# Kernel optimization log

Measured on AMD Instinct MI355X. Metric: run time of the kernel, lower is better.

## Reference

```python
import jax, jax.numpy as jnp
import numpy as np

B, N, D, H, L, C = 64, 64, 64, 256, 64, 2


def setup_inputs() -> dict:
    key = jax.random.key(0)
    ks = iter(jax.random.split(key, 40))

    def p(*shape):
        return (jax.random.normal(next(ks), shape, jnp.float32) / np.sqrt(shape[0])).astype(jnp.float32)

    inp = {
        "x": jax.random.normal(next(ks), (B, N, D), jnp.float32),
        "adj": jax.random.uniform(next(ks), (B, N, N), jnp.float32),
        "condition": jax.random.normal(next(ks), (B, C), jnp.float32),
        # GraphConv layers
        "gc1_W": p(D, H), "gc1_b": jnp.zeros((H,)),
        "gc2_W": p(H, H), "gc2_b": jnp.zeros((H,)),
        "gc3mu_W": p(H, L), "gc3mu_b": jnp.zeros((L,)),
        "gc3lv_W": p(H, L), "gc3lv_b": jnp.zeros((L,)),
        # condition encoder
        "ce_W1": p(C, H), "ce_b1": jnp.zeros((H,)),
        "ce_W2": p(H, H), "ce_b2": jnp.zeros((H,)),
        # decoder
        "dec_W1": p(L + H, H), "dec_b1": jnp.zeros((H,)),
        "dec_W2": p(H, H), "dec_b2": jnp.zeros((H,)),
        "dec_W3": p(H, D), "dec_b3": jnp.zeros((D,)),
        # atom type predictor
        "at_W1": p(D, H), "at_b1": jnp.zeros((H,)),
        "at_W2": p(H, 8), "at_b2": jnp.zeros((8,)),
        # bond predictor
        "bp_W1": p(2 * D + H, H), "bp_b1": jnp.zeros((H,)),
        "bp_W2": p(H, H), "bp_b2": jnp.zeros((H,)),
        "bp_W3": p(H, 4), "bp_b3": jnp.zeros((4,)),
        # rule encoder
        "re_W1": p(D, H), "re_b1": jnp.zeros((H,)),
        "re_W2": p(H, 4), "re_b2": jnp.zeros((4,)),
    }
    return inp


def reference(x, adj, condition,
              gc1_W, gc1_b, gc2_W, gc2_b, gc3mu_W, gc3mu_b, gc3lv_W, gc3lv_b,
              ce_W1, ce_b1, ce_W2, ce_b2,
              dec_W1, dec_b1, dec_W2, dec_b2, dec_W3, dec_b3,
              at_W1, at_b1, at_W2, at_b2,
              bp_W1, bp_b1, bp_W2, bp_b2, bp_W3, bp_b3,
              re_W1, re_b1, re_W2, re_b2):
    relu = jax.nn.relu

    def gc(h, W, b):  # batched GraphConv: adj @ h then linear
        return jnp.einsum('bij,bjd->bid', adj, h) @ W + b

    # encode
    h = relu(gc(x, gc1_W, gc1_b))
    h = relu(gc(h, gc2_W, gc2_b))
    mu = gc(h, gc3mu_W, gc3mu_b)        # [B,N,L]
    logvar = gc(h, gc3lv_W, gc3lv_b)    # [B,N,L]
    z = mu  # eval-mode reparameterize (deterministic)

    # decode: condition encoding broadcast over nodes
    cond = relu(condition @ ce_W1 + ce_b1) @ ce_W2 + ce_b2  # [B,H]
    dec_in = jnp.concatenate([z, jnp.broadcast_to(cond[:, None, :], (z.shape[0], z.shape[1], cond.shape[-1]))], axis=-1)
    f = relu(dec_in @ dec_W1 + dec_b1)
    f = relu(f @ dec_W2 + dec_b2)
    features = jax.nn.sigmoid(f @ dec_W3 + dec_b3)  # [B,N,D]

    type_probs = jax.nn.softmax(relu(features @ at_W1 + at_b1) @ at_W2 + at_b2, axis=-1)  # [B,N,8]
    valence = jax.nn.sigmoid(relu(features @ re_W1 + re_b1) @ re_W2 + re_b2) * 4.0        # [B,N,4]
    atom_features = features * jnp.mean(type_probs, axis=-1, keepdims=True)               # [B,N,D]

    # dense pairwise bond probabilities (vectorized version of the per-pair MLP)
    b, n, d = atom_features.shape
    af_i = jnp.broadcast_to(atom_features[:, :, None, :], (b, n, n, d))
    af_j = jnp.broadcast_to(atom_features[:, None, :, :], (b, n, n, d))
    cnd = jnp.broadcast_to(cond[:, None, None, :], (b, n, n, cond.shape[-1]))
    pair = jnp.concatenate([af_i, af_j, cnd], axis=-1)  # [B,N,N,2D+H]
    g = relu(pair @ bp_W1 + bp_b1)
    g = relu(g @ bp_W2 + bp_b2)
    bond_probs = jax.nn.softmax(g @ bp_W3 + bp_b3, axis=-1)  # [B,N,N,4]

    return (atom_features, bond_probs, valence, mu, logvar)
```

## Files before the change

kernel.cpp:

```cpp
#include <hip/hip_runtime.h>

typedef short short8 __attribute__((ext_vector_type(8)));
typedef float f32x4 __attribute__((ext_vector_type(4)));
typedef unsigned short u16;
typedef unsigned int u32;

__device__ __forceinline__ u16 f2bf(float f) {
  union { float f; u32 u; } x; x.f = f;
  u32 u = x.u;
  u32 r = (u + 0x7FFFu + ((u >> 16) & 1u)) >> 16;
  return (u16)r;
}

__device__ __forceinline__ u32 cvtpk(float lo, float hi) {
  u32 r;
  asm("v_cvt_pk_bf16_f32 %0, %1, %2" : "=v"(r) : "v"(lo), "v"(hi));
  return r;
}

#define OW2T   0
#define OW3TX  65536
#define ODW1A  69632
#define ODW2   86016
#define ODW3   151552
#define OBPA   167936
#define OBPB   184320
#define OREW1  200704
#define OREW2  217088
#define OWMU   221184
#define OWLV   237568

__global__ void __launch_bounds__(512) k_prep(
    const float* __restrict__ cnd, const float* __restrict__ ceW1,
    const float* __restrict__ ceb1, const float* __restrict__ ceW2,
    const float* __restrict__ ceb2, const float* __restrict__ bpW1,
    const float* __restrict__ bpb1, const float* __restrict__ dW1,
    const float* __restrict__ db1, const float* __restrict__ dW2,
    const float* __restrict__ dW3, const float* __restrict__ bpW2,
    const float* __restrict__ bpW3, const float* __restrict__ reW1,
    const float* __restrict__ reW2, const float* __restrict__ gmuW,
    const float* __restrict__ glvW, float* __restrict__ ctf,
    float* __restrict__ ctv, u16* __restrict__ WB) {
  __shared__ float h[256], c2s[256], prf[256], prv[256];
  __shared__ float T[64][65];
  int bid = blockIdx.x, t = threadIdx.x;
  if (bid < 64) {
    int b = bid;
    if (t < 256) {
      float c0 = cnd[b * 2 + 0], c1 = cnd[b * 2 + 1];
      h[t] = fmaxf(c0 * ceW1[t] + c1 * ceW1[256 + t] + ceb1[t], 0.f);
    }
    __syncthreads();
    int col = t & 255, g = t >> 8;
    {
      float acc = 0.f;
      #pragma unroll 8
      for (int k = g * 128; k < g * 128 + 128; k++) acc += h[k] * ceW2[k * 256 + col];
      if (g) prf[col] = acc;
      __syncthreads();
      if (!g) c2s[col] = acc + prf[col] + ceb2[col];
    }
    __syncthreads();
    float af = 0.f, av = 0.f;
    #pragma unroll 4
    for (int k = g * 128; k < g * 128 + 128; k++) {
      float cv = c2s[k];
      af += cv * bpW1[(128 + k) * 256 + col];
      av += cv * dW1[(64 + k) * 256 + col];
    }
    if (g) { prf[col] = af; prv[col] = av; }
    __syncthreads();
    if (!g) {
      ctf[b * 256 + col] = af + prf[col] + bpb1[col];
      ctv[b * 256 + col] = av + prv[col] + db1[col];
    }
    return;
  }
  int mb = bid - 64;
  if (mb >= 60) {
    if (t < 256) {
      const float* s = (mb == 60) ? reW2 : bpW3;
      u16* d = WB + ((mb == 60) ? OREW2 : OW3TX);
      #pragma unroll
      for (int c = 0; c < 16; c++) {
        float v = (c < 4) ? s[t * 4 + c] : 0.f;
        d[c * 256 + t] = f2bf(v);
      }
    }
    return;
  }
  const float* src; u16* dst; int sld, dld, tr, tc; float sc = 1.f;
  if (mb < 4)       { src = dW1;           dst = WB + ODW1A; sld = 256; dld = 64;  tr = 0;            tc = mb;          }
  else if (mb < 20) { int e = mb - 4;  src = dW2;  dst = WB + ODW2; sld = 256; dld = 256; tr = e >> 2; tc = e & 3; }
  else if (mb < 24) { int e = mb - 20; src = dW3;  dst = WB + ODW3; sld = 64;  dld = 256; tr = e;      tc = 0;     }
  else if (mb < 28) { int e = mb - 24; src = bpW1; dst = WB + OBPA; sld = 256; dld = 64;  tr = 0;      tc = e; sc = 0.125f; }
  else if (mb < 32) { int e = mb - 28; src = bpW1 + 64 * 256; dst = WB + OBPB; sld = 256; dld = 64; tr = 0; tc = e; sc = 0.125f; }
  else if (mb < 36) { int e = mb - 32; src = reW1; dst = WB + OREW1; sld = 256; dld = 64; tr = 0;      tc = e;     }
  else if (mb < 40) { int e = mb - 36; src = gmuW; dst = WB + OWMU; sld = 64;  dld = 256; tr = e;      tc = 0;     }
  else if (mb < 44) { int e = mb - 40; src = glvW; dst = WB + OWLV; sld = 64;  dld = 256; tr = e;      tc = 0;     }
  else              { int e = mb - 44; src = bpW2; dst = WB + OW2T; sld = 256; dld = 256; tr = e >> 2; tc = e & 3; }
  int rl = t >> 6, cl = t & 63;
  #pragma unroll
  for (int it = 0; it < 8; it++) {
    int r = it * 8 + rl;
    T[r][cl] = src[(tr * 64 + r) * sld + tc * 64 + cl] * sc;
  }
  __syncthreads();
  #pragma unroll
  for (int it = 0; it < 8; it++) {
    int c2_ = it * 8 + rl;
    dst[(tc * 64 + c2_) * dld + tr * 64 + cl] = f2bf(T[cl][c2_]);
  }
}

__global__ void __launch_bounds__(512) k_gc1(
    const float* __restrict__ adj, const float* __restrict__ x,
    const float* __restrict__ W1, const float* __restrict__ b1,
    float* __restrict__ out) {
  __shared__ float adj_s[64 * 64];
  __shared__ float x_s[64 * 64];
  __shared__ float ax_s[64 * 64];
  __shared__ float h_s[64 * 64];
  int cg = blockIdx.x, b = blockIdx.y, t = threadIdx.x;
  const float* A = adj + b * 4096;
  const float* X = x + b * 4096;
  for (int e = t; e < 4096; e += 512) { adj_s[e] = A[e]; x_s[e] = X[e]; }
  __syncthreads();
  int c = t & 63, rg = t >> 6;
  {
    float acc[8];
    #pragma unroll
    for (int m = 0; m < 8; m++) acc[m] = 0.f;
    #pragma unroll 4
    for (int j4 = 0; j4 < 16; j4++) {
      float xv0 = x_s[(j4 * 4 + 0) * 64 + c];
      float xv1 = x_s[(j4 * 4 + 1) * 64 + c];
      float xv2 = x_s[(j4 * 4 + 2) * 64 + c];
      float xv3 = x_s[(j4 * 4 + 3) * 64 + c];
      #pragma unroll
      for (int m = 0; m < 8; m++) {
        float4 a4 = *(const float4*)&adj_s[(m * 8 + rg) * 64 + j4 * 4];
        acc[m] += a4.x * xv0 + a4.y * xv1 + a4.z * xv2 + a4.w * xv3;
      }
    }
    #pragma unroll
    for (int m = 0; m < 8; m++) ax_s[(m * 8 + rg) * 64 + c] = acc[m];
  }
  __syncthreads();
  {
    float bv = b1[cg * 64 + c];
    float acc[8];
    #pragma unroll
    for (int m = 0; m < 8; m++) acc[m] = bv;
    #pragma unroll 4
    for (int k4 = 0; k4 < 16; k4++) {
      float w0 = W1[(k4 * 4 + 0) * 256 + cg * 64 + c];
      float w1 = W1[(k4 * 4 + 1) * 256 + cg * 64 + c];
      float w2 = W1[(k4 * 4 + 2) * 256 + cg * 64 + c];
      float w3 = W1[(k4 * 4 + 3) * 256 + cg * 64 + c];
      #pragma unroll
      for (int m = 0; m < 8; m++) {
        float4 a4 = *(const float4*)&ax_s[(m * 8 + rg) * 64 + k4 * 4];
        acc[m] += a4.x * w0 + a4.y * w1 + a4.z * w2 + a4.w * w3;
      }
    }
    #pragma unroll
    for (int m = 0; m < 8; m++) h_s[(m * 8 + rg) * 64 + c] = fmaxf(acc[m], 0.f);
  }
  __syncthreads();
  {
    float acc[8];
    #pragma unroll
    for (int m = 0; m < 8; m++) acc[m] = 0.f;
    #pragma unroll 4
    for (int j4 = 0; j4 < 16; j4++) {
      float h0 = h_s[(j4 * 4 + 0) * 64 + c];
      float h1 = h_s[(j4 * 4 + 1) * 64 + c];
      float h2 = h_s[(j4 * 4 + 2) * 64 + c];
      float h3 = h_s[(j4 * 4 + 3) * 64 + c];
      #pragma unroll
      for (int m = 0; m < 8; m++) {
        float4 a4 = *(const float4*)&adj_s[(m * 8 + rg) * 64 + j4 * 4];
        acc[m] += a4.x * h0 + a4.y * h1 + a4.z * h2 + a4.w * h3;
      }
    }
    float* O = out + b * 64 * 256 + cg * 64;
    #pragma unroll
    for (int m = 0; m < 8; m++) O[(m * 8 + rg) * 256 + c] = acc[m];
  }
}

__global__ void __launch_bounds__(512) k_linadj(
    const float* __restrict__ adj, const float* __restrict__ in,
    const float* __restrict__ W, const float* __restrict__ bias,
    float* __restrict__ out) {
  __shared__ float adj_s[64 * 64];
  __shared__ float in_s[32 * 256];
  __shared__ float h_s[64 * 64];
  int cg = blockIdx.x, b = blockIdx.y, t = threadIdx.x;
  const float* A = adj + b * 4096;
  for (int e = t; e < 4096; e += 512) adj_s[e] = A[e];
  int c = t & 63, rg = t >> 6;
  float bv = bias[cg * 64 + c];
  #pragma unroll
  for (int half = 0; half < 2; half++) {
    if (half) __syncthreads();
    const float* I = in + (b * 64 + half * 32) * 256;
    for (int e = t; e < 32 * 256; e += 512) in_s[e] = I[e];
    __syncthreads();
    float acc[4];
    #pragma unroll
    for (int m = 0; m < 4; m++) acc[m] = bv;
    #pragma unroll 4
    for (int k4 = 0; k4 < 64; k4++) {
      float w0 = W[(k4 * 4 + 0) * 256 + cg * 64 + c];
      float w1 = W[(k4 * 4 + 1) * 256 + cg * 64 + c];
      float w2 = W[(k4 * 4 + 2) * 256 + cg * 64 + c];
      float w3 = W[(k4 * 4 + 3) * 256 + cg * 64 + c];
      #pragma unroll
      for (int m = 0; m < 4; m++) {
        float4 i4 = *(const float4*)&in_s[(m * 8 + rg) * 256 + k4 * 4];
        acc[m] += i4.x * w0 + i4.y * w1 + i4.z * w2 + i4.w * w3;
      }
    }
    #pragma unroll
    for (int m = 0; m < 4; m++)
      h_s[(half * 32 + m * 8 + rg) * 64 + c] = fmaxf(acc[m], 0.f);
  }
  __syncthreads();
  {
    float acc[8];
    #pragma unroll
    for (int m = 0; m < 8; m++) acc[m] = 0.f;
    #pragma unroll 4
    for (int j4 = 0; j4 < 16; j4++) {
      float h0 = h_s[(j4 * 4 + 0) * 64 + c];
      float h1 = h_s[(j4 * 4 + 1) * 64 + c];
      float h2 = h_s[(j4 * 4 + 2) * 64 + c];
      float h3 = h_s[(j4 * 4 + 3) * 64 + c];
      #pragma unroll
      for (int m = 0; m < 8; m++) {
        float4 a4 = *(const float4*)&adj_s[(m * 8 + rg) * 64 + j4 * 4];
        acc[m] += a4.x * h0 + a4.y * h1 + a4.z * h2 + a4.w * h3;
      }
    }
    float* O = out + b * 64 * 256 + cg * 64;
    #pragma unroll
    for (int m = 0; m < 8; m++) O[(m * 8 + rg) * 256 + c] = acc[m];
  }
}

template <int KK, int WU, int WV, bool UG, bool VG, int ULEN, int VLEN>
__device__ __forceinline__ void mmrun(const u16* __restrict__ Up, int Uoff,
                                      const u16* __restrict__ Vp, int Voff,
                                      const char* lds, int ut0, int vt0, int lr, int lk,
                                      f32x4 (&acc)[WU][WV]) {
  #pragma unroll
  for (int kk = 0; kk < KK; kk++) {
    short8 uf[WU], vf[WV];
    #pragma unroll
    for (int i = 0; i < WU; i++) {
      int row = (ut0 + i) * 16 + lr;
      if constexpr (UG) {
        uf[i] = *(const short8*)(Up + row * ULEN + kk * 32 + lk * 8);
      } else {
        int byt = Uoff + row * (ULEN * 2) + kk * 64 + lk * 16;
        byt ^= (row & 7) << 4;
        uf[i] = *(const short8*)(lds + byt);
      }
    }
    #pragma unroll
    for (int j = 0; j < WV; j++) {
      int row = (vt0 + j) * 16 + lr;
      if constexpr (VG) {
        vf[j] = *(const short8*)(Vp + row * VLEN + kk * 32 + lk * 8);
      } else {
        int byt = Voff + row * (VLEN * 2) + kk * 64 + lk * 16;
        byt ^= (row & 7) << 4;
        vf[j] = *(const short8*)(lds + byt);
      }
    }
    #pragma unroll
    for (int i = 0; i < WU; i++)
      #pragma unroll
      for (int j = 0; j < WV; j++)
        acc[i][j] = __builtin_amdgcn_mfma_f32_16x16x32_bf16(uf[i], vf[j], acc[i][j], 0, 0, 0);
  }
}

__device__ __forceinline__ void st64(char* lds, int off, int rowlen, int crow, int ccol0,
                                     float a0, float a1, float a2, float a3) {
  uint2 pk; pk.x = cvtpk(a0, a1); pk.y = cvtpk(a2, a3);
  int byt = off + crow * (rowlen * 2) + ccol0 * 2;
  byt ^= (crow & 7) << 4;
  *(uint2*)(lds + byt) = pk;
}

template <int WU, int WV>
__device__ __forceinline__ void zacc(f32x4 (&acc)[WU][WV]) {
  #pragma unroll
  for (int i = 0; i < WU; i++)
    #pragma unroll
    for (int j = 0; j < WV; j++) acc[i][j] = (f32x4){0.f, 0.f, 0.f, 0.f};
}

__global__ void __launch_bounds__(1024) k_chain2(
    const u16* __restrict__ WB, const float* __restrict__ ah2_g,
    const float* __restrict__ ctv, const float* __restrict__ ctf,
    const float* __restrict__ gmub, const float* __restrict__ glvb,
    const float* __restrict__ db2, const float* __restrict__ db3,
    const float* __restrict__ reb1, const float* __restrict__ reb2,
    float* __restrict__ mu_out, float* __restrict__ lv_out,
    float* __restrict__ af_out, float* __restrict__ val_out,
    float* __restrict__ P, float* __restrict__ Q) {
  __shared__ char L[65536];
  constexpr int S2 = 0, S3 = 32768;
  int b = blockIdx.x, t = threadIdx.x;
  int w = t >> 6, lane = t & 63, lr = lane & 15, lk = lane >> 4;

  {
    int r = t >> 4, cb = (t & 15) * 16;
    #pragma unroll
    for (int q = 0; q < 4; q++) {
      float4 v = *(const float4*)(ah2_g + ((b * 64 + r) * 256 + cb + q * 4));
      st64(L, S2, 256, r, cb + q * 4, v.x, v.y, v.z, v.w);
    }
  }
  __syncthreads();
  {
    f32x4 a[2][1]; zacc(a);
    int sel = w >> 3, wq = w & 7;
    int ut0 = (wq & 1) * 2, vt = wq >> 1;
    const u16* Up = WB + (sel ? OWLV : OWMU);
    mmrun<8, 2, 1, true, false, 256, 256>(Up, 0, WB, S2, L, ut0, vt, lr, lk, a);
    int crow = vt * 16 + lr;
    const float* bb = sel ? glvb : gmub;
    float* gout = sel ? lv_out : mu_out;
    #pragma unroll
    for (int i = 0; i < 2; i++) {
      int cc = (ut0 + i) * 16 + lk * 4;
      float4 bv = *(const float4*)(bb + cc);
      float o0 = a[i][0][0] + bv.x, o1 = a[i][0][1] + bv.y;
      float o2 = a[i][0][2] + bv.z, o3 = a[i][0][3] + bv.w;
      *(float4*)(gout + ((b * 64 + crow) * 64 + cc)) = make_float4(o0, o1, o2, o3);
      if (sel == 0) st64(L, S3, 64, crow, cc, o0, o1, o2, o3);
    }
  }
  __syncthreads();
  {
    f32x4 a[2][2]; zacc(a);
    int ut0 = (w & 7) * 2, vt0 = (w >> 3) * 2;
    mmrun<2, 2, 2, true, false, 64, 64>(WB + ODW1A, 0, WB, S3, L, ut0, vt0, lr, lk, a);
    #pragma unroll
    for (int j = 0; j < 2; j++) {
      int crow = (vt0 + j) * 16 + lr;
      #pragma unroll
      for (int i = 0; i < 2; i++) {
        int cc = (ut0 + i) * 16 + lk * 4;
        float4 cv = *(const float4*)(ctv + b * 256 + cc);
        st64(L, S2, 256, crow, cc, fmaxf(a[i][j][0] + cv.x, 0.f), fmaxf(a[i][j][1] + cv.y, 0.f),
             fmaxf(a[i][j][2] + cv.z, 0.f), fmaxf(a[i][j][3] + cv.w, 0.f));
      }
    }
  }
  __syncthreads();
  {
    f32x4 a[2][2]; zacc(a);
    int ut0 = (w & 7) * 2, vt0 = (w >> 3) * 2;
    mmrun<8, 2, 2, true, false, 256, 256>(WB + ODW2, 0, WB, S2, L, ut0, vt0, lr, lk, a);
    #pragma unroll
    for (int j = 0; j < 2; j++) {
      int crow = (vt0 + j) * 16 + lr;
      #pragma unroll
      for (int i = 0; i < 2; i++) {
        int cc = (ut0 + i) * 16 + lk * 4;
        float4 bv = *(const float4*)(db2 + cc);
        st64(L, S3, 256, crow, cc, fmaxf(a[i][j][0] + bv.x, 0.f), fmaxf(a[i][j][1] + bv.y, 0.f),
             fmaxf(a[i][j][2] + bv.z, 0.f), fmaxf(a[i][j][3] + bv.w, 0.f));
      }
    }
  }
  __syncthreads();
  {
    f32x4 a[1][1]; zacc(a);
    int ut = w & 3, vt = w >> 2;
    mmrun<8, 1, 1, true, false, 256, 256>(WB + ODW3, 0, WB, S3, L, ut, vt, lr, lk, a);
    int crow = vt * 16 + lr, cc = ut * 16 + lk * 4;
    float4 bv = *(const float4*)(db3 + cc);
    float s0 = 1.f / (1.f + expf(-(a[0][0][0] + bv.x)));
    float s1 = 1.f / (1.f + expf(-(a[0][0][1] + bv.y)));
    float s2 = 1.f / (1.f + expf(-(a[0][0][2] + bv.z)));
    float s3 = 1.f / (1.f + expf(-(a[0][0][3] + bv.w)));
    *(float4*)(af_out + ((b * 64 + crow) * 64 + cc)) =
        make_float4(s0 * 0.125f, s1 * 0.125f, s2 * 0.125f, s3 * 0.125f);
    st64(L, S2, 64, crow, cc, s0, s1, s2, s3);
  }
  __syncthreads();
  {
    f32x4 a[2][4]; zacc(a);
    int ut0 = (w & 7) * 2;
    int sel = w >> 3;
    const u16* Up = WB + (sel ? OBPB : OBPA);
    mmrun<2, 2, 4, true, false, 64, 64>(Up, 0, WB, S2, L, ut0, 0, lr, lk, a);
    float* out = sel ? Q : P;
    #pragma unroll
    for (int i = 0; i < 2; i++) {
      int cc = (ut0 + i) * 16 + lk * 4;
      float4 cv = make_float4(0.f, 0.f, 0.f, 0.f);
      if (sel == 0) cv = *(const float4*)(ctf + b * 256 + cc);
      #pragma unroll
      for (int j = 0; j < 4; j++) {
        int crow = j * 16 + lr;
        *(float4*)(out + ((b * 64 + crow) * 256 + cc)) =
            make_float4(a[i][j][0] + cv.x, a[i][j][1] + cv.y, a[i][j][2] + cv.z, a[i][j][3] + cv.w);
      }
    }
  }
  {
    f32x4 a[2][2]; zacc(a);
    int ut0 = (w & 7) * 2, vt0 = (w >> 3) * 2;
    mmrun<2, 2, 2, true, false, 64, 64>(WB + OREW1, 0, WB, S2, L, ut0, vt0, lr, lk, a);
    #pragma unroll
    for (int j = 0; j < 2; j++) {
      int crow = (vt0 + j) * 16 + lr;
      #pragma unroll
      for (int i = 0; i < 2; i++) {
        int cc = (ut0 + i) * 16 + lk * 4;
        float4 bv = *(const float4*)(reb1 + cc);
        st64(L, S3, 256, crow, cc, fmaxf(a[i][j][0] + bv.x, 0.f), fmaxf(a[i][j][1] + bv.y, 0.f),
             fmaxf(a[i][j][2] + bv.z, 0.f), fmaxf(a[i][j][3] + bv.w, 0.f));
      }
    }
  }
  __syncthreads();
  if (w < 4) {
    f32x4 a[1][1]; zacc(a);
    mmrun<8, 1, 1, true, false, 256, 256>(WB + OREW2, 0, WB, S3, L, 0, w, lr, lk, a);
    if (lk == 0) {
      float4 rb = *(const float4*)reb2;
      float v0 = 4.f / (1.f + expf(-(a[0][0][0] + rb.x)));
      float v1 = 4.f / (1.f + expf(-(a[0][0][1] + rb.y)));
      float v2 = 4.f / (1.f + expf(-(a[0][0][2] + rb.z)));
      float v3 = 4.f / (1.f + expf(-(a[0][0][3] + rb.w)));
      *(float4*)(val_out + (b * 64 + w * 16 + lr) * 4) = make_float4(v0, v1, v2, v3);
    }
  }
}

__global__ void __launch_bounds__(512, 4) k_bond(
    const float* __restrict__ P, const float* __restrict__ Q,
    const u16* __restrict__ W2T, const float* __restrict__ b2,
    const u16* __restrict__ W3Tx, const float* __restrict__ b3,
    float* __restrict__ bp_out) {
  __shared__ u16 G[2 * 64 * 256];
  int flat = blockIdx.x;
  int xcd = flat & 7, rest = flat >> 3;
  int b = xcd * 8 + (rest >> 5);
  int i0 = (rest & 31) * 2;
  int t = threadIdx.x;
  int lane = t & 63, w = t >> 6;
  int lr = lane & 15, lk = lane >> 4;

  {
    int colg = t & 63, rq = t >> 6;
    const float* Pb = P + (b * 64 + i0) * 256 + colg * 4;
    float4 p0 = *(const float4*)(Pb);
    float4 p1 = *(const float4*)(Pb + 256);
    const float* Qb = Q + b * 64 * 256;
    #pragma unroll
    for (int r = rq * 8; r < rq * 8 + 8; r++) {
      float4 q4 = *(const float4*)(Qb + r * 256 + colg * 4);
      int byt = (r * 512 + colg * 8) ^ ((r & 7) << 4);
      uint2 pk0, pk1;
      pk0.x = cvtpk(fmaxf(p0.x + q4.x, 0.f), fmaxf(p0.y + q4.y, 0.f));
      pk0.y = cvtpk(fmaxf(p0.z + q4.z, 0.f), fmaxf(p0.w + q4.w, 0.f));
      pk1.x = cvtpk(fmaxf(p1.x + q4.x, 0.f), fmaxf(p1.y + q4.y, 0.f));
      pk1.y = cvtpk(fmaxf(p1.z + q4.z, 0.f), fmaxf(p1.w + q4.w, 0.f));
      *(uint2*)((char*)G + byt) = pk0;
      *(uint2*)((char*)G + 32768 + byt) = pk1;
    }
  }
  __syncthreads();

  f32x4 acc[2][2][4];
  #pragma unroll
  for (int tl = 0; tl < 2; tl++)
    #pragma unroll
    for (int ni = 0; ni < 2; ni++)
      #pragma unroll
      for (int mi = 0; mi < 4; mi++) acc[tl][ni][mi] = (f32x4){0.f, 0.f, 0.f, 0.f};

  const u16* Wl = W2T + (w * 32 + lr) * 256 + lk * 8;
  short8 bwc0 = *(const short8*)(Wl);
  short8 bwc1 = *(const short8*)(Wl + 16 * 256);
  for (int kk = 0; kk < 8; kk++) {
    int kn = (kk + 1) & 7;
    short8 bwn0 = *(const short8*)(Wl + kn * 32);
    short8 bwn1 = *(const short8*)(Wl + 16 * 256 + kn * 32);
    __builtin_amdgcn_s_setprio(1);
    #pragma unroll
    for (int mi = 0; mi < 4; mi++) {
      int row = mi * 16 + lr;
      int byt = (row * 512 + kk * 64 + lk * 16) ^ ((row & 7) << 4);
      short8 a0 = *(const short8*)((const char*)G + byt);
      short8 a1 = *(const short8*)((const char*)G + 32768 + byt);
      acc[0][0][mi] = __builtin_amdgcn_mfma_f32_16x16x32_bf16(bwc0, a0, acc[0][0][mi], 0, 0, 0);
      acc[1][0][mi] = __builtin_amdgcn_mfma_f32_16x16x32_bf16(bwc0, a1, acc[1][0][mi], 0, 0, 0);
      acc[0][1][mi] = __builtin_amdgcn_mfma_f32_16x16x32_bf16(bwc1, a0, acc[0][1][mi], 0, 0, 0);
      acc[1][1][mi] = __builtin_amdgcn_mfma_f32_16x16x32_bf16(bwc1, a1, acc[1][1][mi], 0, 0, 0);
    }
    __builtin_amdgcn_s_setprio(0);
    bwc0 = bwn0;
    bwc1 = bwn1;
  }
  __syncthreads();

  #pragma unroll
  for (int tl = 0; tl < 2; tl++)
    #pragma unroll
    for (int ni = 0; ni < 2; ni++) {
      int col0 = w * 32 + ni * 16 + lk * 4;
      float4 bb = *(const float4*)(b2 + col0);
      #pragma unroll
      for (int mi = 0; mi < 4; mi++) {
        int grow = mi * 16 + lr;
        uint2 pk;
        pk.x = cvtpk(fmaxf(acc[tl][ni][mi][0] + bb.x, 0.f), fmaxf(acc[tl][ni][mi][1] + bb.y, 0.f));
        pk.y = cvtpk(fmaxf(acc[tl][ni][mi][2] + bb.z, 0.f), fmaxf(acc[tl][ni][mi][3] + bb.w, 0.f));
        int byt = ((grow * 512 + col0 * 2) ^ ((grow & 7) << 4)) + tl * 32768;
        *(uint2*)((char*)G + byt) = pk;
      }
    }
  __syncthreads();

  f32x4 acc2[2][4];
  #pragma unroll
  for (int tl = 0; tl < 2; tl++)
    #pragma unroll
    for (int mi = 0; mi < 4; mi++) acc2[tl][mi] = (f32x4){0.f, 0.f, 0.f, 0.f};
  {
    short8 bw2 = *(const short8*)(W3Tx + lr * 256 + w * 32 + lk * 8);
    #pragma unroll
    for (int tl = 0; tl < 2; tl++)
      #pragma unroll
      for (int mi = 0; mi < 4; mi++) {
        int row = mi * 16 + lr;
        int byt = ((row * 512 + (w * 32 + lk * 8) * 2) ^ ((row & 7) << 4)) + tl * 32768;
        short8 a = *(const short8*)((const char*)G + byt);
        acc2[tl][mi] = __builtin_amdgcn_mfma_f32_16x16x32_bf16(a, bw2, acc2[tl][mi], 0, 0, 0);
      }
  }
  __syncthreads();
  float* pf = (float*)G;
  if (lr < 4) {
    #pragma unroll
    for (int tl = 0; tl < 2; tl++)
      #pragma unroll
      for (int mi = 0; mi < 4; mi++)
        #pragma unroll
        for (int rg = 0; rg < 4; rg++) {
          int row = mi * 16 + lk * 4 + rg;
          pf[tl * 8192 + (w * 64 + row) * 4 + lr] = acc2[tl][mi][rg];
        }
  }
  __syncthreads();

  {
    int tl = t >> 8, idx = t & 255;
    int r = idx >> 2, c = idx & 3;
    float lv = b3[c];
    #pragma unroll
    for (int wq = 0; wq < 8; wq++) lv += pf[tl * 8192 + (wq * 64 + r) * 4 + c];
    float m = fmaxf(lv, __shfl_xor(lv, 1));
    m = fmaxf(m, __shfl_xor(m, 2));
    float e = expf(lv - m);
    float s = e + __shfl_xor(e, 1);
    s += __shfl_xor(s, 2);
    bp_out[((b * 64 + i0 + tl) * 64 + r) * 4 + c] = e / s;
  }
}

extern "C" void kernel_launch(void* const* d_in, const int* in_sizes, int n_in,
                              void* d_out, int out_size, void* d_ws, size_t ws_size,
                              hipStream_t stream) {
  const float* x    = (const float*)d_in[0];
  const float* adj  = (const float*)d_in[1];
  const float* cnd  = (const float*)d_in[2];
  const float* gc1W = (const float*)d_in[3];
  const float* gc1b = (const float*)d_in[4];
  const float* gc2W = (const float*)d_in[5];
  const float* gc2b = (const float*)d_in[6];
  const float* gmuW = (const float*)d_in[7];
  const float* gmub = (const float*)d_in[8];
  const float* glvW = (const float*)d_in[9];
  const float* glvb = (const float*)d_in[10];
  const float* ceW1 = (const float*)d_in[11];
  const float* ceb1 = (const float*)d_in[12];
  const float* ceW2 = (const float*)d_in[13];
  const float* ceb2 = (const float*)d_in[14];
  const float* dW1  = (const float*)d_in[15];
  const float* db1  = (const float*)d_in[16];
  const float* dW2  = (const float*)d_in[17];
  const float* db2  = (const float*)d_in[18];
  const float* dW3  = (const float*)d_in[19];
  const float* db3  = (const float*)d_in[20];
  const float* bpW1 = (const float*)d_in[25];
  const float* bpb1 = (const float*)d_in[26];
  const float* bpW2 = (const float*)d_in[27];
  const float* bpb2 = (const float*)d_in[28];
  const float* bpW3 = (const float*)d_in[29];
  const float* bpb3 = (const float*)d_in[30];
  const float* reW1 = (const float*)d_in[31];
  const float* reb1 = (const float*)d_in[32];
  const float* reW2 = (const float*)d_in[33];
  const float* reb2 = (const float*)d_in[34];

  float* out = (float*)d_out;
  float* af_out  = out;
  float* bp_out  = out + 262144;
  float* val_out = out + 1310720;
  float* mu_out  = out + 1327104;
  float* lv_out  = out + 1589248;

  float* ws   = (float*)d_ws;
  float* ctf  = ws;
  float* ctv  = ws + 16384;
  float* buf1 = ws + 49152;
  float* buf2 = buf1 + 1048576;
  float* buf3 = buf2 + 1048576;
  u16*   WB   = (u16*)(buf3 + 1048576);

  k_prep<<<126, 512, 0, stream>>>(cnd, ceW1, ceb1, ceW2, ceb2, bpW1, bpb1, dW1, db1,
                                  dW2, dW3, bpW2, bpW3, reW1, reW2, gmuW, glvW,
                                  ctf, ctv, WB);
  k_gc1<<<dim3(4, 64), 512, 0, stream>>>(adj, x, gc1W, gc1b, buf3);
  k_linadj<<<dim3(4, 64), 512, 0, stream>>>(adj, buf3, gc2W, gc2b, buf1);
  k_chain2<<<64, 1024, 0, stream>>>(WB, buf1, ctv, ctf, gmub, glvb, db2, db3,
                                    reb1, reb2, mu_out, lv_out, af_out, val_out,
                                    buf2, buf3);
  k_bond<<<2048, 512, 0, stream>>>(buf2, buf3, WB + OW2T, bpb2, WB + OW3TX, bpb3, bp_out);
}
```

Measured before the change: 153.4 us.

## Merge prep and gc1 kernels into one launch; restructure bond final-layer softmax

The weight-prep/condition kernel and the first GraphConv kernel become one launch of 382 blocks, branching on block index and sharing a 64KB shared buffer. This removes one kernel launch and lets the two independent jobs run at the same time. In the bond kernel, the final 256->4 MFMA is now split across waves by (tile, row block) with the full K loop inside each wave. The softmax is done in registers with shuffles, which removes the shared-memory partial-sum pass and two barriers. The cost is more K-loop MFMAs per wave and lanes lr>=4 doing redundant softmax work.

```diff
diff --git a/kernel.cpp b/kernel.cpp
--- a/kernel.cpp
+++ b/kernel.cpp
@@ -30,7 +30,7 @@
 #define OWMU   221184
 #define OWLV   237568
 
-__global__ void __launch_bounds__(512) k_prep(
+__global__ void __launch_bounds__(512) k_pg(
     const float* __restrict__ cnd, const float* __restrict__ ceW1,
     const float* __restrict__ ceb1, const float* __restrict__ ceW2,
     const float* __restrict__ ceb2, const float* __restrict__ bpW1,
@@ -39,89 +39,93 @@
     const float* __restrict__ dW3, const float* __restrict__ bpW2,
     const float* __restrict__ bpW3, const float* __restrict__ reW1,
     const float* __restrict__ reW2, const float* __restrict__ gmuW,
-    const float* __restrict__ glvW, float* __restrict__ ctf,
-    float* __restrict__ ctv, u16* __restrict__ WB) {
-  __shared__ float h[256], c2s[256], prf[256], prv[256];
-  __shared__ float T[64][65];
+    const float* __restrict__ glvW, const float* __restrict__ adj,
+    const float* __restrict__ x, const float* __restrict__ gc1W,
+    const float* __restrict__ gc1b, float* __restrict__ ctf,
+    float* __restrict__ ctv, u16* __restrict__ WB, float* __restrict__ ah1_out) {
+  __shared__ char SM[65536];
   int bid = blockIdx.x, t = threadIdx.x;
-  if (bid < 64) {
-    int b = bid;
-    if (t < 256) {
-      float c0 = cnd[b * 2 + 0], c1 = cnd[b * 2 + 1];
-      h[t] = fmaxf(c0 * ceW1[t] + c1 * ceW1[256 + t] + ceb1[t], 0.f);
+  if (bid < 126) {
+    float* h   = (float*)SM;
+    float* c2s = h + 256;
+    float* prf = h + 512;
+    float* prv = h + 768;
+    float (*T)[65] = (float(*)[65])(SM + 4096);
+    if (bid < 64) {
+      int b = bid;
+      if (t < 256) {
+        float c0 = cnd[b * 2 + 0], c1 = cnd[b * 2 + 1];
+        h[t] = fmaxf(c0 * ceW1[t] + c1 * ceW1[256 + t] + ceb1[t], 0.f);
+      }
+      __syncthreads();
+      int col = t & 255, g = t >> 8;
+      {
+        float acc = 0.f;
+        #pragma unroll 8
+        for (int k = g * 128; k < g * 128 + 128; k++) acc += h[k] * ceW2[k * 256 + col];
+        if (g) prf[col] = acc;
+        __syncthreads();
+        if (!g) c2s[col] = acc + prf[col] + ceb2[col];
+      }
+      __syncthreads();
+      float af = 0.f, av = 0.f;
+      #pragma unroll 4
+      for (int k = g * 128; k < g * 128 + 128; k++) {
+        float cv = c2s[k];
+        af += cv * bpW1[(128 + k) * 256 + col];
+        av += cv * dW1[(64 + k) * 256 + col];
+      }
+      if (g) { prf[col] = af; prv[col] = av; }
+      __syncthreads();
+      if (!g) {
+        ctf[b * 256 + col] = af + prf[col] + bpb1[col];
+        ctv[b * 256 + col] = av + prv[col] + db1[col];
+      }
+      return;
+    }
+    int mb = bid - 64;
+    if (mb >= 60) {
+      if (t < 256) {
+        const float* s = (mb == 60) ? reW2 : bpW3;
+        u16* d = WB + ((mb == 60) ? OREW2 : OW3TX);
+        #pragma unroll
+        for (int c = 0; c < 16; c++) {
+          float v = (c < 4) ? s[t * 4 + c] : 0.f;
+          d[c * 256 + t] = f2bf(v);
+        }
+      }
+      return;
+    }
+    const float* src; u16* dst; int sld, dld, tr, tc; float sc = 1.f;
+    if (mb < 4)       { src = dW1;           dst = WB + ODW1A; sld = 256; dld = 64;  tr = 0;            tc = mb;          }
+    else if (mb < 20) { int e = mb - 4;  src = dW2;  dst = WB + ODW2; sld = 256; dld = 256; tr = e >> 2; tc = e & 3; }
+    else if (mb < 24) { int e = mb - 20; src = dW3;  dst = WB + ODW3; sld = 64;  dld = 256; tr = e;      tc = 0;     }
+    else if (mb < 28) { int e = mb - 24; src = bpW1; dst = WB + OBPA; sld = 256; dld = 64;  tr = 0;      tc = e; sc = 0.125f; }
+    else if (mb < 32) { int e = mb - 28; src = bpW1 + 64 * 256; dst = WB + OBPB; sld = 256; dld = 64; tr = 0; tc = e; sc = 0.125f; }
+    else if (mb < 36) { int e = mb - 32; src = reW1; dst = WB + OREW1; sld = 256; dld = 64; tr = 0;      tc = e;     }
+    else if (mb < 40) { int e = mb - 36; src = gmuW; dst = WB + OWMU; sld = 64;  dld = 256; tr = e;      tc = 0;     }
+    else if (mb < 44) { int e = mb - 40; src = glvW; dst = WB + OWLV; sld = 64;  dld = 256; tr = e;      tc = 0;     }
+    else              { int e = mb - 44; src = bpW2; dst = WB + OW2T; sld = 256; dld = 256; tr = e >> 2; tc = e & 3; }
+    int rl = t >> 6, cl = t & 63;
+    #pragma unroll
+    for (int it = 0; it < 8; it++) {
+      int r = it * 8 + rl;
+      T[r][cl] = src[(tr * 64 + r) * sld + tc * 64 + cl] * sc;
     }
     __syncthreads();
-    int col = t & 255, g = t >> 8;
-    {
-      float acc = 0.f;
-      #pragma unroll 8
-      for (int k = g * 128; k < g * 128 + 128; k++) acc += h[k] * ceW2[k * 256 + col];
-      if (g) prf[col] = acc;
-      __syncthreads();
-      if (!g) c2s[col] = acc + prf[col] + ceb2[col];
-    }
-    __syncthreads();
-    float af = 0.f, av = 0.f;
-    #pragma unroll 4
-    for (int k = g * 128; k < g * 128 + 128; k++) {
-      float cv = c2s[k];
-      af += cv * bpW1[(128 + k) * 256 + col];
-      av += cv * dW1[(64 + k) * 256 + col];
-    }
-    if (g) { prf[col] = af; prv[col] = av; }
-    __syncthreads();
-    if (!g) {
-      ctf[b * 256 + col] = af + prf[col] + bpb1[col];
-      ctv[b * 256 + col] = av + prv[col] + db1[col];
+    #pragma unroll
+    for (int it = 0; it < 8; it++) {
+      int c2_ = it * 8 + rl;
+      dst[(tc * 64 + c2_) * dld + tr * 64 + cl] = f2bf(T[cl][c2_]);
     }
     return;
   }
-  int mb = bid - 64;
-  if (mb >= 60) {
-    if (t < 256) {
-      const float* s = (mb == 60) ? reW2 : bpW3;
-      u16* d = WB + ((mb == 60) ? OREW2 : OW3TX);
-      #pragma unroll
-      for (int c = 0; c < 16; c++) {
-        float v = (c < 4) ? s[t * 4 + c] : 0.f;
-        d[c * 256 + t] = f2bf(v);
-      }
-    }
-    return;
-  }
-  const float* src; u16* dst; int sld, dld, tr, tc; float sc = 1.f;
-  if (mb < 4)       { src = dW1;           dst = WB + ODW1A; sld = 256; dld = 64;  tr = 0;            tc = mb;          }
-  else if (mb < 20) { int e = mb - 4;  src = dW2;  dst = WB + ODW2; sld = 256; dld = 256; tr = e >> 2; tc = e & 3; }
-  else if (mb < 24) { int e = mb - 20; src = dW3;  dst = WB + ODW3; sld = 64;  dld = 256; tr = e;      tc = 0;     }
-  else if (mb < 28) { int e = mb - 24; src = bpW1; dst = WB + OBPA; sld = 256; dld = 64;  tr = 0;      tc = e; sc = 0.125f; }
-  else if (mb < 32) { int e = mb - 28; src = bpW1 + 64 * 256; dst = WB + OBPB; sld = 256; dld = 64; tr = 0; tc = e; sc = 0.125f; }
-  else if (mb < 36) { int e = mb - 32; src = reW1; dst = WB + OREW1; sld = 256; dld = 64; tr = 0;      tc = e;     }
-  else if (mb < 40) { int e = mb - 36; src = gmuW; dst = WB + OWMU; sld = 64;  dld = 256; tr = e;      tc = 0;     }
-  else if (mb < 44) { int e = mb - 40; src = glvW; dst = WB + OWLV; sld = 64;  dld = 256; tr = e;      tc = 0;     }
-  else              { int e = mb - 44; src = bpW2; dst = WB + OW2T; sld = 256; dld = 256; tr = e >> 2; tc = e & 3; }
-  int rl = t >> 6, cl = t & 63;
-  #pragma unroll
-  for (int it = 0; it < 8; it++) {
-    int r = it * 8 + rl;
-    T[r][cl] = src[(tr * 64 + r) * sld + tc * 64 + cl] * sc;
-  }
-  __syncthreads();
-  #pragma unroll
-  for (int it = 0; it < 8; it++) {
-    int c2_ = it * 8 + rl;
-    dst[(tc * 64 + c2_) * dld + tr * 64 + cl] = f2bf(T[cl][c2_]);
-  }
-}
-
-__global__ void __launch_bounds__(512) k_gc1(
-    const float* __restrict__ adj, const float* __restrict__ x,
-    const float* __restrict__ W1, const float* __restrict__ b1,
-    float* __restrict__ out) {
-  __shared__ float adj_s[64 * 64];
-  __shared__ float x_s[64 * 64];
-  __shared__ float ax_s[64 * 64];
-  __shared__ float h_s[64 * 64];
-  int cg = blockIdx.x, b = blockIdx.y, t = threadIdx.x;
+  int e2 = bid - 126;
+  int cg = e2 & 3, b = e2 >> 2;
+  float* adj_s = (float*)SM;
+  float* x_s   = adj_s + 4096;
+  float* ax_s  = adj_s + 8192;
+  float* h_s   = adj_s + 12288;
   const float* A = adj + b * 4096;
   const float* X = x + b * 4096;
   for (int e = t; e < 4096; e += 512) { adj_s[e] = A[e]; x_s[e] = X[e]; }
@@ -148,16 +152,16 @@
   }
   __syncthreads();
   {
-    float bv = b1[cg * 64 + c];
+    float bv = gc1b[cg * 64 + c];
     float acc[8];
     #pragma unroll
     for (int m = 0; m < 8; m++) acc[m] = bv;
     #pragma unroll 4
     for (int k4 = 0; k4 < 16; k4++) {
-      float w0 = W1[(k4 * 4 + 0) * 256 + cg * 64 + c];
-      float w1 = W1[(k4 * 4 + 1) * 256 + cg * 64 + c];
-      float w2 = W1[(k4 * 4 + 2) * 256 + cg * 64 + c];
-      float w3 = W1[(k4 * 4 + 3) * 256 + cg * 64 + c];
+      float w0 = gc1W[(k4 * 4 + 0) * 256 + cg * 64 + c];
+      float w1 = gc1W[(k4 * 4 + 1) * 256 + cg * 64 + c];
+      float w2 = gc1W[(k4 * 4 + 2) * 256 + cg * 64 + c];
+      float w3 = gc1W[(k4 * 4 + 3) * 256 + cg * 64 + c];
       #pragma unroll
       for (int m = 0; m < 8; m++) {
         float4 a4 = *(const float4*)&ax_s[(m * 8 + rg) * 64 + k4 * 4];
@@ -184,7 +188,7 @@
         acc[m] += a4.x * h0 + a4.y * h1 + a4.z * h2 + a4.w * h3;
       }
     }
-    float* O = out + b * 64 * 256 + cg * 64;
+    float* O = ah1_out + b * 64 * 256 + cg * 64;
     #pragma unroll
     for (int m = 0; m < 8; m++) O[(m * 8 + rg) * 256 + c] = acc[m];
   }
@@ -533,50 +537,36 @@
     }
   __syncthreads();
 
-  f32x4 acc2[2][4];
-  #pragma unroll
-  for (int tl = 0; tl < 2; tl++)
-    #pragma unroll
-    for (int mi = 0; mi < 4; mi++) acc2[tl][mi] = (f32x4){0.f, 0.f, 0.f, 0.f};
-  {
-    short8 bw2 = *(const short8*)(W3Tx + lr * 256 + w * 32 + lk * 8);
-    #pragma unroll
-    for (int tl = 0; tl < 2; tl++)
-      #pragma unroll
-      for (int mi = 0; mi < 4; mi++) {
-        int row = mi * 16 + lr;
-        int byt = ((row * 512 + (w * 32 + lk * 8) * 2) ^ ((row & 7) << 4)) + tl * 32768;
-        short8 a = *(const short8*)((const char*)G + byt);
-        acc2[tl][mi] = __builtin_amdgcn_mfma_f32_16x16x32_bf16(a, bw2, acc2[tl][mi], 0, 0, 0);
-      }
-  }
-  __syncthreads();
-  float* pf = (float*)G;
-  if (lr < 4) {
-    #pragma unroll
-    for (int tl = 0; tl < 2; tl++)
-      #pragma unroll
-      for (int mi = 0; mi < 4; mi++)
-        #pragma unroll
-        for (int rg = 0; rg < 4; rg++) {
-          int row = mi * 16 + lk * 4 + rg;
-          pf[tl * 8192 + (w * 64 + row) * 4 + lr] = acc2[tl][mi][rg];
-        }
-  }
-  __syncthreads();
-
-  {
-    int tl = t >> 8, idx = t & 255;
-    int r = idx >> 2, c = idx & 3;
-    float lv = b3[c];
-    #pragma unroll
-    for (int wq = 0; wq < 8; wq++) lv += pf[tl * 8192 + (wq * 64 + r) * 4 + c];
-    float m = fmaxf(lv, __shfl_xor(lv, 1));
-    m = fmaxf(m, __shfl_xor(m, 2));
-    float e = expf(lv - m);
-    float s = e + __shfl_xor(e, 1);
-    s += __shfl_xor(s, 2);
-    bp_out[((b * 64 + i0 + tl) * 64 + r) * 4 + c] = e / s;
+  {
+    int tl2 = w & 1, mi = w >> 1;
+    f32x4 acc2 = (f32x4){0.f, 0.f, 0.f, 0.f};
+    #pragma unroll
+    for (int kk2 = 0; kk2 < 8; kk2++) {
+      short8 bw2 = *(const short8*)(W3Tx + lr * 256 + kk2 * 32 + lk * 8);
+      int row = mi * 16 + lr;
+      int byt = ((row * 512 + (kk2 * 32 + lk * 8) * 2) ^ ((row & 7) << 4)) + tl2 * 32768;
+      short8 a = *(const short8*)((const char*)G + byt);
+      acc2 = __builtin_amdgcn_mfma_f32_16x16x32_bf16(a, bw2, acc2, 0, 0, 0);
+    }
+    float b3v = b3[lr & 3];
+    float res[4];
+    #pragma unroll
+    for (int rg = 0; rg < 4; rg++) {
+      float v = acc2[rg] + b3v;
+      float m = fmaxf(v, __shfl_xor(v, 1));
+      m = fmaxf(m, __shfl_xor(m, 2));
+      float e = expf(v - m);
+      float s = e + __shfl_xor(e, 1);
+      s += __shfl_xor(s, 2);
+      res[rg] = e / s;
+    }
+    if (lr < 4) {
+      #pragma unroll
+      for (int rg = 0; rg < 4; rg++) {
+        int row = mi * 16 + lk * 4 + rg;
+        bp_out[((b * 64 + i0 + tl2) * 64 + row) * 4 + lr] = res[rg];
+      }
+    }
   }
 }
 
@@ -630,10 +620,9 @@
   float* buf3 = buf2 + 1048576;
   u16*   WB   = (u16*)(buf3 + 1048576);
 
-  k_prep<<<126, 512, 0, stream>>>(cnd, ceW1, ceb1, ceW2, ceb2, bpW1, bpb1, dW1, db1,
-                                  dW2, dW3, bpW2, bpW3, reW1, reW2, gmuW, glvW,
-                                  ctf, ctv, WB);
-  k_gc1<<<dim3(4, 64), 512, 0, stream>>>(adj, x, gc1W, gc1b, buf3);
+  k_pg<<<382, 512, 0, stream>>>(cnd, ceW1, ceb1, ceW2, ceb2, bpW1, bpb1, dW1, db1,
+                                dW2, dW3, bpW2, bpW3, reW1, reW2, gmuW, glvW,
+                                adj, x, gc1W, gc1b, ctf, ctv, WB, buf3);
   k_linadj<<<dim3(4, 64), 512, 0, stream>>>(adj, buf3, gc2W, gc2b, buf1);
   k_chain2<<<64, 1024, 0, stream>>>(WB, buf1, ctv, ctf, gmub, glvb, db2, db3,
                                     reb1, reb2, mu_out, lv_out, af_out, val_out,
```

After: 152.6 us. No clear change (-0.5%).
